# Kernel tuning notes

Measured on AMD Instinct MI355X. Metric: run time of the kernel, lower is better.

## Reference

```python
import jax, jax.numpy as jnp
import numpy as np

B, T, V, H, L = 64, 256, 128, 1024, 2


def setup_inputs() -> dict:
    key = jax.random.key(0)
    ks = jax.random.split(key, 11)
    s = 0.02
    return {
        "x": jax.random.normal(ks[0], (B, T, V), jnp.float32),
        "h": jax.random.normal(ks[1], (L, B, H), jnp.float32),
        "c": jax.random.normal(ks[2], (L, B, H), jnp.float32),
        "Wih0": jax.random.normal(ks[3], (4 * H, V), jnp.float32) * s,
        "Whh0": jax.random.normal(ks[4], (4 * H, H), jnp.float32) * s,
        "bih0": jax.random.normal(ks[5], (4 * H,), jnp.float32) * s,
        "bhh0": jax.random.normal(ks[6], (4 * H,), jnp.float32) * s,
        "Wih1": jax.random.normal(ks[7], (4 * H, H), jnp.float32) * s,
        "Whh1": jax.random.normal(ks[8], (4 * H, H), jnp.float32) * s,
        "bih1": jax.random.normal(ks[9], (4 * H,), jnp.float32) * s,
        "bhh1": jax.random.normal(ks[10], (4 * H,), jnp.float32) * s,
    }


def _lstm_cell(x_in, h_prev, c_prev, Wih, Whh, bih, bhh):
    # z: (B, 4H); gate order i, f, g, o (torch.nn.LSTMCell convention)
    z = x_in @ Wih.T + bih + h_prev @ Whh.T + bhh
    i, f, g, o = jnp.split(z, 4, axis=-1)
    c_new = jax.nn.sigmoid(f) * c_prev + jax.nn.sigmoid(i) * jnp.tanh(g)
    h_new = jax.nn.sigmoid(o) * jnp.tanh(c_new)
    return h_new, c_new


def reference(x, h, c, Wih0, Whh0, bih0, bhh0, Wih1, Whh1, bih1, bhh1):
    Wih = (Wih0, Wih1)
    Whh = (Whh0, Whh1)
    bih = (bih0, bih1)
    bhh = (bhh0, bhh1)

    def step(carry, x_t):
        h_c, c_c = carry  # each (L, B, H)
        inp = x_t  # (B, V)
        hs, cs = [], []
        for i in range(L):
            h_new, c_new = _lstm_cell(inp, h_c[i], c_c[i], Wih[i], Whh[i], bih[i], bhh[i])
            hs.append(h_new)
            cs.append(c_new)
            inp = h_new
        return (jnp.stack(hs, 0), jnp.stack(cs, 0)), inp  # emit top-layer h

    (h_f, c_f), outs_tbm = jax.lax.scan(step, (h, c), jnp.swapaxes(x, 0, 1))
    outs = jnp.swapaxes(outs_tbm, 0, 1)  # (B, T, H)
    return outs, h_f, c_f
```

## Files before the change

### kernel.cpp

```cpp
#include <hip/hip_runtime.h>
#include <stdint.h>

#define TSTEPS 256
#define KB0  36
#define KB1  64

#define WPK0_OFF 0ull
#define WPK1_OFF 9437184ull
#define A0_OFF   26214400ull
#define A1_OFF   63963136ull
#define BIAS_OFF 131072000ull
#define FLG_OFF  131104768ull

typedef __attribute__((ext_vector_type(8))) short bf16x8;
typedef __attribute__((ext_vector_type(4))) float f32x4;

__device__ __forceinline__ unsigned short f2bf(float x) {
  unsigned int u = __float_as_uint(x);
  u = (u + 0x7FFFu + ((u >> 16) & 1u)) >> 16;
  return (unsigned short)u;
}

__device__ __forceinline__ int kpos(int k) {
  return (((k & 15) >> 2) << 3) + (((k >> 4) & 1) << 2) + (k & 3);
}
__device__ __forceinline__ int kpos4(int k) {
  return (((k & 15) >> 2) << 3) + (((k >> 4) & 1) << 2);
}

__device__ __forceinline__ float sigm(float z) {
  return 1.0f / (1.0f + __expf(-z));
}

__device__ __forceinline__ void spin1(unsigned int* p, unsigned int tgt) {
  while (__hip_atomic_load(p, __ATOMIC_RELAXED, __HIP_MEMORY_SCOPE_AGENT) < tgt)
    __builtin_amdgcn_s_sleep(4);
}

__global__ void k_init(const float* __restrict__ bih0, const float* __restrict__ bhh0,
                       const float* __restrict__ bih1, const float* __restrict__ bhh1,
                       float* __restrict__ bias, unsigned int* __restrict__ flg) {
  int i = blockIdx.x * 256 + threadIdx.x;
  flg[i] = 0u;
  if (i < 4096) {
    bias[i]        = bih0[i] + bhh0[i];
    bias[4096 + i] = bih1[i] + bhh1[i];
  }
}

__global__ void k_packW(const float* __restrict__ Wih, const float* __restrict__ Whh,
                        const int Kih, const int KB, unsigned short* __restrict__ dst) {
  const int K = KB << 5;
  const int total = K << 12;
  int i = blockIdx.x * 256 + threadIdx.x;
  if (i >= total) return;
  int n = i / K, k = i - n * K;
  float w = (k < Kih) ? Wih[n * Kih + k] : Whh[n * 1024 + (k - Kih)];
  int gt = n >> 10, hcol = n & 1023;
  int wgi = hcol >> 3, j = hcol & 7;
  int nt = gt >> 1;
  int l15 = ((gt & 1) << 3) | j;
  int kb = k >> 5;
  size_t idx = ((size_t)((wgi * 2 + nt) * KB + kb) << 9) + (l15 << 5) + kpos(k & 31);
  dst[idx] = f2bf(w);
}

__global__ void k_packX(const float* __restrict__ x, unsigned short* __restrict__ a0) {
  int i = blockIdx.x * 256 + threadIdx.x;
  int v = i & 127, t = (i >> 7) & 255, b = i >> 15;
  a0[(size_t)t * 73728 + (size_t)(((v >> 5) << 6) + b) * 32 + kpos(v & 31)] = f2bf(x[i]);
}

__global__ void k_packH(const float* __restrict__ h,
                        unsigned short* __restrict__ a0, unsigned short* __restrict__ a1) {
  int i = blockIdx.x * 256 + threadIdx.x;
  int l = i >> 16, b = (i >> 10) & 63, hc = i & 1023;
  unsigned short v = f2bf(h[i]);
  if (l == 0) {
    int k = 128 + hc;
    a0[(size_t)(((k >> 5) << 6) + b) * 32 + kpos(k & 31)] = v;
  } else {
    int k = 1024 + hc;
    a1[(size_t)(((k >> 5) << 6) + b) * 32 + kpos(k & 31)] = v;
  }
}

template <int LAYER>
__device__ __forceinline__ void run_layer(
    const int wg, const int tid,
    const float* __restrict__ c_in, float* __restrict__ out,
    const unsigned short* __restrict__ W,
    unsigned short* __restrict__ a0, unsigned short* __restrict__ a1,
    const float* __restrict__ bias,
    unsigned int* flags0, unsigned int* flags1,
    unsigned short* ldsw, float (*h_lds)[8]) {
  constexpr int KB = LAYER ? KB1 : KB0;
  constexpr int AELEM = KB * 2048;

  const int lane = tid & 63, wv = tid >> 6;
  const int l15 = lane & 15, lg = lane >> 4;
  const int lbo = lane * 8;

  const unsigned short* Ard = LAYER ? a1 : a0;

  {
    const unsigned short* Wg = W + (size_t)(wg * 2) * KB * 512;
    for (int i = tid; i < KB * 128; i += 256) {
      int u = i & 63;
      *(bf16x8*)(ldsw + (size_t)((((i >> 6) << 6) | ((u & 3) << 4) | (u >> 2)) * 8)) =
          *(const bf16x8*)(Wg + (size_t)i * 8);
    }
  }

  const int arowoff = (wv * 16 + l15) * 32 + lg * 8;

  const int hc = wg * 8 + l15;
  const int brow = wv * 16 + lg * 4;
  float cc[4];
  float bgi = 0.f, bgf = 0.f, bgg = 0.f, bgo = 0.f;
  if (l15 < 8) {
#pragma unroll
    for (int r = 0; r < 4; ++r)
      cc[r] = c_in[LAYER * 65536 + (brow + r) * 1024 + hc];
    bgi = bias[LAYER * 4096 + 0 * 1024 + hc];
    bgf = bias[LAYER * 4096 + 1 * 1024 + hc];
    bgg = bias[LAYER * 4096 + 2 * 1024 + hc];
    bgo = bias[LAYER * 4096 + 3 * 1024 + hc];
  }

  const int db = tid >> 1;
  const int dc0 = (tid & 1) * 4;
  const int dhc = wg * 8 + dc0;

  unsigned int* myflag = (LAYER ? flags1 : flags0) + wg * 32;
  __syncthreads();

  for (int t = 0; t < TSTEPS; ++t) {
    if (LAYER == 0) {
      if (t && tid < 128) spin1(flags0 + tid * 32, (unsigned int)t);
    } else {
      if (tid < 128) spin1(flags0 + tid * 32, (unsigned int)(t + 1));
      else if (t)    spin1(flags1 + (tid - 128) * 32, (unsigned int)t);
    }
    __syncthreads();

    const unsigned long long* Ab64 =
        (const unsigned long long*)(Ard + (size_t)t * AELEM + arowoff);
    f32x4 acc[2][2];
    acc[0][0] = (f32x4){0.f, 0.f, 0.f, 0.f};
    acc[0][1] = (f32x4){0.f, 0.f, 0.f, 0.f};
    acc[1][0] = (f32x4){0.f, 0.f, 0.f, 0.f};
    acc[1][1] = (f32x4){0.f, 0.f, 0.f, 0.f};
#pragma unroll
    for (int kb = 0; kb < KB; ++kb) {
      union { unsigned long long u[2]; bf16x8 v; } a;
      a.u[0] = __hip_atomic_load(Ab64 + (size_t)kb * 512 + 0,
                                 __ATOMIC_RELAXED, __HIP_MEMORY_SCOPE_AGENT);
      a.u[1] = __hip_atomic_load(Ab64 + (size_t)kb * 512 + 1,
                                 __ATOMIC_RELAXED, __HIP_MEMORY_SCOPE_AGENT);
      bf16x8 b0 = *(const bf16x8*)(ldsw + (size_t)kb * 512 + lbo);
      bf16x8 b1 = *(const bf16x8*)(ldsw + (size_t)(KB + kb) * 512 + lbo);
      acc[0][kb & 1] =
          __builtin_amdgcn_mfma_f32_16x16x32_bf16(a.v, b0, acc[0][kb & 1], 0, 0, 0);
      acc[1][kb & 1] =
          __builtin_amdgcn_mfma_f32_16x16x32_bf16(a.v, b1, acc[1][kb & 1], 0, 0, 0);
    }
    f32x4 z0 = acc[0][0] + acc[0][1];
    f32x4 z1 = acc[1][0] + acc[1][1];

    f32x4 zf, zo;
#pragma unroll
    for (int r = 0; r < 4; ++r) {
      zf[r] = __shfl_xor(z0[r], 8, 64);
      zo[r] = __shfl_xor(z1[r], 8, 64);
    }

    if (l15 < 8) {
#pragma unroll
      for (int r = 0; r < 4; ++r) {
        float iv = sigm(z0[r] + bgi);
        float fv = sigm(zf[r] + bgf);
        float gv = tanhf(z1[r] + bgg);
        float ov = sigm(zo[r] + bgo);
        cc[r] = fv * cc[r] + iv * gv;
        h_lds[brow + r][l15] = ov * tanhf(cc[r]);
      }
    }
    __syncthreads();

    if (tid < 128) {
      float4 hf = *(const float4*)&h_lds[db][dc0];
      unsigned long long pk =
          (unsigned long long)(((unsigned int)f2bf(hf.y) << 16) | f2bf(hf.x)) |
          ((unsigned long long)(((unsigned int)f2bf(hf.w) << 16) | f2bf(hf.z)) << 32);
      if (LAYER == 0) {
        int k = dhc;
        __hip_atomic_store(
            (unsigned long long*)(a1 + (size_t)t * 131072 +
                                  (size_t)(((k >> 5) << 6) + db) * 32 + kpos4(k)),
            pk, __ATOMIC_RELAXED, __HIP_MEMORY_SCOPE_AGENT);
        if (t < TSTEPS - 1) {
          int k2 = 128 + dhc;
          __hip_atomic_store(
              (unsigned long long*)(a0 + (size_t)(t + 1) * 73728 +
                                    (size_t)(((k2 >> 5) << 6) + db) * 32 + kpos4(k2)),
              pk, __ATOMIC_RELAXED, __HIP_MEMORY_SCOPE_AGENT);
        }
      } else {
        *(float4*)(out + ((size_t)db * 256 + t) * 1024 + dhc) = hf;
        if (t < TSTEPS - 1) {
          int k = 1024 + dhc;
          __hip_atomic_store(
              (unsigned long long*)(a1 + (size_t)(t + 1) * 131072 +
                                    (size_t)(((k >> 5) << 6) + db) * 32 + kpos4(k)),
              pk, __ATOMIC_RELAXED, __HIP_MEMORY_SCOPE_AGENT);
        }
      }
      if (t == TSTEPS - 1)
        *(float4*)(out + 16777216ull + (size_t)LAYER * 65536 +
                   (size_t)db * 1024 + dhc) = hf;
    }
    if (t == TSTEPS - 1 && l15 < 8) {
#pragma unroll
      for (int r = 0; r < 4; ++r)
        out[16777216ull + 131072ull + (size_t)LAYER * 65536 +
            (size_t)(brow + r) * 1024 + hc] = cc[r];
    }

    __syncthreads();
    if (tid == 0)
      __hip_atomic_store(myflag, (unsigned int)(t + 1), __ATOMIC_RELAXED,
                         __HIP_MEMORY_SCOPE_AGENT);
  }
}

__global__ __launch_bounds__(256, 1) void lstm_main(
    const float* __restrict__ c_in, float* __restrict__ out,
    const unsigned short* __restrict__ wpk0, const unsigned short* __restrict__ wpk1,
    unsigned short* a0, unsigned short* a1,
    const float* __restrict__ bias, unsigned int* flg) {
  __shared__ unsigned short ldsw[KB1 * 1024];
  __shared__ float h_lds[64][8];
  int bid = blockIdx.x, tid = threadIdx.x;
  unsigned int* flags0 = flg;
  unsigned int* flags1 = flg + 4096;
  if (bid < 128)
    run_layer<0>(bid, tid, c_in, out, wpk0, a0, a1, bias, flags0, flags1, ldsw, h_lds);
  else
    run_layer<1>(bid - 128, tid, c_in, out, wpk1, a0, a1, bias, flags0, flags1, ldsw, h_lds);
}

extern "C" void kernel_launch(void* const* d_in, const int* in_sizes, int n_in,
                              void* d_out, int out_size, void* d_ws, size_t ws_size,
                              hipStream_t stream) {
  const float* x    = (const float*)d_in[0];
  const float* h    = (const float*)d_in[1];
  const float* c    = (const float*)d_in[2];
  const float* Wih0 = (const float*)d_in[3];
  const float* Whh0 = (const float*)d_in[4];
  const float* bih0 = (const float*)d_in[5];
  const float* bhh0 = (const float*)d_in[6];
  const float* Wih1 = (const float*)d_in[7];
  const float* Whh1 = (const float*)d_in[8];
  const float* bih1 = (const float*)d_in[9];
  const float* bhh1 = (const float*)d_in[10];

  char* ws = (char*)d_ws;
  unsigned short* wpk0 = (unsigned short*)(ws + WPK0_OFF);
  unsigned short* wpk1 = (unsigned short*)(ws + WPK1_OFF);
  unsigned short* a0   = (unsigned short*)(ws + A0_OFF);
  unsigned short* a1   = (unsigned short*)(ws + A1_OFF);
  float* bias          = (float*)(ws + BIAS_OFF);
  unsigned int* flg    = (unsigned int*)(ws + FLG_OFF);
  float* out = (float*)d_out;

  k_init<<<32, 256, 0, stream>>>(bih0, bhh0, bih1, bhh1, bias, flg);
  k_packW<<<18432, 256, 0, stream>>>(Wih0, Whh0, 128, KB0, wpk0);
  k_packW<<<32768, 256, 0, stream>>>(Wih1, Whh1, 1024, KB1, wpk1);
  k_packX<<<8192, 256, 0, stream>>>(x, a0);
  k_packH<<<512, 256, 0, stream>>>(h, a0, a1);
  lstm_main<<<256, 256, 0, stream>>>(c, out, wpk0, wpk1, a0, a1, bias, flg);
}
```

Measured before the change: 3.076 ms.

## Use acquire fence and plain vector loads for recurrent A operand, pack pairs

The per-step A-operand loads change from two relaxed 64-bit atomic loads to one plain 128-bit vector load. Visibility is now guaranteed by an acquire load on the workgroup's flag plus an extra barrier at each step. The pack kernels now handle two elements per thread and write packed 32-bit atomic stores, halving grid sizes. The spin sleep interval is shortened. The aim is fewer, wider memory instructions in the latency-critical recurrent loop, at the risk that the acquire-on-own-flag fence does not reliably order reads of other blocks' data.

```diff
diff --git a/kernel.cpp b/kernel.cpp
--- a/kernel.cpp
+++ b/kernel.cpp
@@ -32,56 +32,69 @@
   return 1.0f / (1.0f + __expf(-z));
 }
 
+__device__ __forceinline__ void st_u32(unsigned int* p, unsigned int v) {
+  __hip_atomic_store(p, v, __ATOMIC_RELAXED, __HIP_MEMORY_SCOPE_AGENT);
+}
+__device__ __forceinline__ void st_f32(float* p, float v) {
+  __hip_atomic_store(p, v, __ATOMIC_RELAXED, __HIP_MEMORY_SCOPE_AGENT);
+}
+
 __device__ __forceinline__ void spin1(unsigned int* p, unsigned int tgt) {
   while (__hip_atomic_load(p, __ATOMIC_RELAXED, __HIP_MEMORY_SCOPE_AGENT) < tgt)
-    __builtin_amdgcn_s_sleep(4);
+    __builtin_amdgcn_s_sleep(2);
 }
 
 __global__ void k_init(const float* __restrict__ bih0, const float* __restrict__ bhh0,
                        const float* __restrict__ bih1, const float* __restrict__ bhh1,
                        float* __restrict__ bias, unsigned int* __restrict__ flg) {
   int i = blockIdx.x * 256 + threadIdx.x;
-  flg[i] = 0u;
+  st_u32(flg + i, 0u);
   if (i < 4096) {
-    bias[i]        = bih0[i] + bhh0[i];
-    bias[4096 + i] = bih1[i] + bhh1[i];
+    st_f32(bias + i,        bih0[i] + bhh0[i]);
+    st_f32(bias + 4096 + i, bih1[i] + bhh1[i]);
   }
 }
 
 __global__ void k_packW(const float* __restrict__ Wih, const float* __restrict__ Whh,
                         const int Kih, const int KB, unsigned short* __restrict__ dst) {
-  const int K = KB << 5;
-  const int total = K << 12;
+  const int K = KB << 5, Kh = K >> 1;
+  const int total = K << 11;
   int i = blockIdx.x * 256 + threadIdx.x;
   if (i >= total) return;
-  int n = i / K, k = i - n * K;
-  float w = (k < Kih) ? Wih[n * Kih + k] : Whh[n * 1024 + (k - Kih)];
+  int n = i / Kh, kp = i - n * Kh, k = kp << 1;
+  float w0 = (k < Kih) ? Wih[n * Kih + k] : Whh[n * 1024 + (k - Kih)];
+  float w1 = (k + 1 < Kih) ? Wih[n * Kih + k + 1] : Whh[n * 1024 + (k + 1 - Kih)];
   int gt = n >> 10, hcol = n & 1023;
   int wgi = hcol >> 3, j = hcol & 7;
   int nt = gt >> 1;
   int l15 = ((gt & 1) << 3) | j;
   int kb = k >> 5;
   size_t idx = ((size_t)((wgi * 2 + nt) * KB + kb) << 9) + (l15 << 5) + kpos(k & 31);
-  dst[idx] = f2bf(w);
+  st_u32((unsigned int*)(dst + idx),
+         ((unsigned int)f2bf(w1) << 16) | f2bf(w0));
 }
 
 __global__ void k_packX(const float* __restrict__ x, unsigned short* __restrict__ a0) {
   int i = blockIdx.x * 256 + threadIdx.x;
-  int v = i & 127, t = (i >> 7) & 255, b = i >> 15;
-  a0[(size_t)t * 73728 + (size_t)(((v >> 5) << 6) + b) * 32 + kpos(v & 31)] = f2bf(x[i]);
+  int v = (i & 63) << 1, t = (i >> 6) & 255, b = i >> 14;
+  const float* xp = x + (size_t)b * 32768 + t * 128 + v;
+  size_t idx = (size_t)t * 73728 + (size_t)(((v >> 5) << 6) + b) * 32 + kpos(v & 31);
+  st_u32((unsigned int*)(a0 + idx),
+         ((unsigned int)f2bf(xp[1]) << 16) | f2bf(xp[0]));
 }
 
 __global__ void k_packH(const float* __restrict__ h,
                         unsigned short* __restrict__ a0, unsigned short* __restrict__ a1) {
   int i = blockIdx.x * 256 + threadIdx.x;
-  int l = i >> 16, b = (i >> 10) & 63, hc = i & 1023;
-  unsigned short v = f2bf(h[i]);
+  int l = i >> 15, b = (i >> 9) & 63, hc = (i & 511) << 1;
+  const float* hp = h + (size_t)l * 65536 + (size_t)b * 1024 + hc;
+  unsigned int pk = ((unsigned int)f2bf(hp[1]) << 16) | f2bf(hp[0]);
   if (l == 0) {
     int k = 128 + hc;
-    a0[(size_t)(((k >> 5) << 6) + b) * 32 + kpos(k & 31)] = v;
+    st_u32((unsigned int*)(a0 + (size_t)(((k >> 5) << 6) + b) * 32 + kpos(k & 31)), pk);
   } else {
     int k = 1024 + hc;
-    a1[(size_t)(((k >> 5) << 6) + b) * 32 + kpos(k & 31)] = v;
+    st_u32((unsigned int*)(a1 + (size_t)(((k >> 5) << 6) + b) * 32 + kpos(k & 31)), pk);
   }
 }
 
@@ -102,6 +115,11 @@
   const int lbo = lane * 8;
 
   const unsigned short* Ard = LAYER ? a1 : a0;
+  unsigned int* myflag = (LAYER ? flags1 : flags0) + wg * 32;
+
+  if (tid == 0)
+    (void)__hip_atomic_load(myflag, __ATOMIC_ACQUIRE, __HIP_MEMORY_SCOPE_AGENT);
+  __syncthreads();
 
   {
     const unsigned short* Wg = W + (size_t)(wg * 2) * KB * 512;
@@ -132,7 +150,6 @@
   const int dc0 = (tid & 1) * 4;
   const int dhc = wg * 8 + dc0;
 
-  unsigned int* myflag = (LAYER ? flags1 : flags0) + wg * 32;
   __syncthreads();
 
   for (int t = 0; t < TSTEPS; ++t) {
@@ -143,9 +160,11 @@
       else if (t)    spin1(flags1 + (tid - 128) * 32, (unsigned int)t);
     }
     __syncthreads();
-
-    const unsigned long long* Ab64 =
-        (const unsigned long long*)(Ard + (size_t)t * AELEM + arowoff);
+    if (tid == 0)
+      (void)__hip_atomic_load(myflag, __ATOMIC_ACQUIRE, __HIP_MEMORY_SCOPE_AGENT);
+    __syncthreads();
+
+    const bf16x8* Af = (const bf16x8*)(Ard + (size_t)t * AELEM + arowoff);
     f32x4 acc[2][2];
     acc[0][0] = (f32x4){0.f, 0.f, 0.f, 0.f};
     acc[0][1] = (f32x4){0.f, 0.f, 0.f, 0.f};
@@ -153,17 +172,13 @@
     acc[1][1] = (f32x4){0.f, 0.f, 0.f, 0.f};
 #pragma unroll
     for (int kb = 0; kb < KB; ++kb) {
-      union { unsigned long long u[2]; bf16x8 v; } a;
-      a.u[0] = __hip_atomic_load(Ab64 + (size_t)kb * 512 + 0,
-                                 __ATOMIC_RELAXED, __HIP_MEMORY_SCOPE_AGENT);
-      a.u[1] = __hip_atomic_load(Ab64 + (size_t)kb * 512 + 1,
-                                 __ATOMIC_RELAXED, __HIP_MEMORY_SCOPE_AGENT);
+      bf16x8 av = Af[(size_t)kb * 256];
       bf16x8 b0 = *(const bf16x8*)(ldsw + (size_t)kb * 512 + lbo);
       bf16x8 b1 = *(const bf16x8*)(ldsw + (size_t)(KB + kb) * 512 + lbo);
       acc[0][kb & 1] =
-          __builtin_amdgcn_mfma_f32_16x16x32_bf16(a.v, b0, acc[0][kb & 1], 0, 0, 0);
+          __builtin_amdgcn_mfma_f32_16x16x32_bf16(av, b0, acc[0][kb & 1], 0, 0, 0);
       acc[1][kb & 1] =
-          __builtin_amdgcn_mfma_f32_16x16x32_bf16(a.v, b1, acc[1][kb & 1], 0, 0, 0);
+          __builtin_amdgcn_mfma_f32_16x16x32_bf16(av, b1, acc[1][kb & 1], 0, 0, 0);
     }
     f32x4 z0 = acc[0][0] + acc[0][1];
     f32x4 z1 = acc[1][0] + acc[1][1];
@@ -275,9 +290,9 @@
   float* out = (float*)d_out;
 
   k_init<<<32, 256, 0, stream>>>(bih0, bhh0, bih1, bhh1, bias, flg);
-  k_packW<<<18432, 256, 0, stream>>>(Wih0, Whh0, 128, KB0, wpk0);
-  k_packW<<<32768, 256, 0, stream>>>(Wih1, Whh1, 1024, KB1, wpk1);
-  k_packX<<<8192, 256, 0, stream>>>(x, a0);
-  k_packH<<<512, 256, 0, stream>>>(h, a0, a1);
+  k_packW<<<9216, 256, 0, stream>>>(Wih0, Whh0, 128, KB0, wpk0);
+  k_packW<<<16384, 256, 0, stream>>>(Wih1, Whh1, 1024, KB1, wpk1);
+  k_packX<<<4096, 256, 0, stream>>>(x, a0);
+  k_packH<<<256, 256, 0, stream>>>(h, a0, a1);
   lstm_main<<<256, 256, 0, stream>>>(c, out, wpk0, wpk1, a0, a1, bias, flg);
 }
```

Result: slower. 3.231 ms (+5.0%).
